# Kernel tuning notes

Measured on AMD Instinct MI355X. Metric: run time of the kernel, lower is better.

Reference implementation:

```python
import jax, jax.numpy as jnp
import numpy as np

DIM = 768
HEADS = 12
HEAD_DIM = DIM // HEADS


def setup_inputs() -> dict:
    key = jax.random.key(0)
    ks = jax.random.split(key, 5)
    s = 0.02
    return {
        "x": jax.random.normal(ks[0], (2, 4096, DIM), dtype=jnp.float32),
        "w_qkv": jax.random.normal(ks[1], (DIM, 3 * DIM), dtype=jnp.float32) * s,
        "b_qkv": jax.random.normal(ks[2], (3 * DIM,), dtype=jnp.float32) * s,
        "w_proj": jax.random.normal(ks[3], (DIM, DIM), dtype=jnp.float32) * s,
        "b_proj": jax.random.normal(ks[4], (DIM,), dtype=jnp.float32) * s,
    }


def reference(x, w_qkv, b_qkv, w_proj, b_proj):
    B, N, _ = x.shape
    scale = HEAD_DIM ** (-0.5)
    qkv = x @ w_qkv + b_qkv                              # [B, N, 3*DIM]
    q, k, v = jnp.split(qkv, 3, axis=-1)
    # 'b n (h d) -> b h n d'
    def to_heads(t):
        return t.reshape(B, N, HEADS, HEAD_DIM).transpose(0, 2, 1, 3)
    q, k, v = to_heads(q), to_heads(k), to_heads(v)
    attn = jnp.einsum('bhnd,bhmd->bhnm', q, k) * scale   # [B, H, N, N]
    attn = jax.nn.softmax(attn, axis=-1)
    out = jnp.einsum('bhnm,bhmd->bhnd', attn, v)         # [B, H, N, D]
    out = out.transpose(0, 2, 1, 3).reshape(B, N, DIM)   # 'b h n d -> b n (h d)'
    return out @ w_proj + b_proj
```

## Files before the change

### kernel.cpp

```cpp
#include <hip/hip_runtime.h>
#include <hip/hip_bf16.h>
#include <stdint.h>

typedef _Float16 f16x8 __attribute__((ext_vector_type(8)));
typedef _Float16 f16x4 __attribute__((ext_vector_type(4)));
typedef uint32_t u32x2 __attribute__((ext_vector_type(2)));
typedef uint32_t u32x4 __attribute__((ext_vector_type(4)));
typedef float floatx4 __attribute__((ext_vector_type(4)));

#define NSEQ 4096
#define DIMM 768
#define NHEADS 12
#define HD 64

__device__ __forceinline__ void gload_lds16(const void* g, void* l) {
  typedef __attribute__((address_space(1))) const uint32_t GQ;
  typedef __attribute__((address_space(3))) uint32_t LQ;
  __builtin_amdgcn_global_load_lds((GQ*)g, (LQ*)l, 16, 0, 0);
}

__device__ __forceinline__ uint16_t f16_bits(float v) {
  _Float16 h = (_Float16)v;
  return __builtin_bit_cast(uint16_t, h);
}

__device__ __forceinline__ uint32_t pkrtz(float a, float b) {
  return __builtin_bit_cast(uint32_t, __builtin_amdgcn_cvt_pkrtz(a, b));
}

__device__ __forceinline__ int swz(int row, int e) {
  return row * 64 + ((((e >> 3) ^ (row & 7)) << 3) | (e & 7));
}

__global__ __launch_bounds__(256) void prologue(
    const float* __restrict__ w0, const float* __restrict__ w1,
    uint16_t* __restrict__ d0, uint16_t* __restrict__ d1,
    const float4* __restrict__ xsrc, f16x8* __restrict__ xdst, int n8) {
  const int z = blockIdx.z;
  const int tx = threadIdx.x, ty = threadIdx.y;
  if (z == 2) {
    const int nthr = 72 * 24 * 256;
    int i = (blockIdx.y * 72 + blockIdx.x) * 256 + ty * 32 + tx;
    for (; i < n8; i += nthr) {
      const float4 a = xsrc[2 * i], b = xsrc[2 * i + 1];
      f16x8 o;
      o[0] = (_Float16)a.x; o[1] = (_Float16)a.y; o[2] = (_Float16)a.z; o[3] = (_Float16)a.w;
      o[4] = (_Float16)b.x; o[5] = (_Float16)b.y; o[6] = (_Float16)b.z; o[7] = (_Float16)b.w;
      xdst[i] = o;
    }
    return;
  }
  __shared__ uint16_t tile[32][33];
  if (z && blockIdx.x >= 24) return;
  const float* src = z ? w1 : w0;
  uint16_t* dst = z ? d1 : d0;
  const int C = z ? 768 : 2304;
  const int R = 768;
  const int c0 = blockIdx.x * 32, r0 = blockIdx.y * 32;
#pragma unroll
  for (int i = 0; i < 32; i += 8)
    tile[ty + i][tx] = f16_bits(src[(size_t)(r0 + ty + i) * C + (c0 + tx)]);
  __syncthreads();
#pragma unroll
  for (int i = 0; i < 32; i += 8)
    dst[(size_t)(c0 + ty + i) * R + (r0 + tx)] = tile[tx][ty + i];
}

__global__ __launch_bounds__(256) void gemm_bt(
    const _Float16* __restrict__ A, const _Float16* __restrict__ Bt,
    const float* __restrict__ bias, int K, int mode, int nbx,
    void* __restrict__ o0, _Float16* __restrict__ o1, _Float16* __restrict__ o2) {
  __shared__ __attribute__((aligned(16))) _Float16 As[3][128 * 32];
  __shared__ __attribute__((aligned(16))) _Float16 Bs[3][128 * 32];
  __shared__ float bias_s[128];
  const int tid = threadIdx.x;
  const int wv = tid >> 6;
  const int lane = tid & 63;
  const int quad = lane >> 4, l16 = lane & 15;
  const int wm = (wv >> 1) * 64, wn = (wv & 1) * 64;
  const int bid = blockIdx.x;
  const int xcd = bid & 7, idx = bid >> 3;
  const int by = xcd * 8 + (idx & 7);
  const int bx = idx >> 3;
  const int m0 = by * 128, n0 = bx * 128;
  (void)nbx;

  if (tid < 128) bias_s[tid] = bias[n0 + tid];

  floatx4 acc[4][4];
#pragma unroll
  for (int i = 0; i < 4; ++i)
#pragma unroll
    for (int j = 0; j < 4; ++j) acc[i][j] = (floatx4){0.f, 0.f, 0.f, 0.f};

  const int gr = lane >> 2, gc = (lane & 3) * 8;
  const _Float16* Ag = A + (size_t)(m0 + wv * 32 + gr) * K + gc;
  const _Float16* Bg = Bt + (size_t)(n0 + wv * 32 + gr) * K + gc;
  const size_t K16 = (size_t)16 * K;

  auto STAGE = [&](int buf, int kt) {
    _Float16* As0 = &As[buf][wv * 1024];
    _Float16* Bs0 = &Bs[buf][wv * 1024];
    gload_lds16(Ag + kt, As0);
    gload_lds16(Ag + kt + K16, As0 + 512);
    gload_lds16(Bg + kt, Bs0);
    gload_lds16(Bg + kt + K16, Bs0 + 512);
  };
  auto COMPUTE = [&](int buf) {
    f16x8 af[4], bfr[4];
#pragma unroll
    for (int i = 0; i < 4; ++i)
      af[i] = *(const f16x8*)&As[buf][(wm + i * 16 + l16) * 32 + quad * 8];
#pragma unroll
    for (int j = 0; j < 4; ++j)
      bfr[j] = *(const f16x8*)&Bs[buf][(wn + j * 16 + l16) * 32 + quad * 8];
    __builtin_amdgcn_s_setprio(1);
#pragma unroll
    for (int i = 0; i < 4; ++i)
#pragma unroll
      for (int j = 0; j < 4; ++j)
        acc[i][j] = __builtin_amdgcn_mfma_f32_16x16x32_f16(af[i], bfr[j], acc[i][j], 0, 0, 0);
    __builtin_amdgcn_s_setprio(0);
  };

  STAGE(0, 0);
  STAGE(1, 32);
  const int nt = K >> 5;
  int b0 = 0, b1 = 1, b2 = 2;
#pragma unroll 1
  for (int t = 0; t < nt - 2; ++t) {
    asm volatile("s_waitcnt vmcnt(4)" ::: "memory");
    __builtin_amdgcn_s_barrier();
    STAGE(b2, (t + 2) * 32);
    COMPUTE(b0);
    const int tmp = b0; b0 = b1; b1 = b2; b2 = tmp;
  }
  asm volatile("s_waitcnt vmcnt(4)" ::: "memory");
  __builtin_amdgcn_s_barrier();
  COMPUTE(b0);
  b0 = b1;
  asm volatile("s_waitcnt vmcnt(0)" ::: "memory");
  __builtin_amdgcn_s_barrier();
  COMPUTE(b0);

  if (mode == 0) {
    float* of = (float*)o0;
#pragma unroll
    for (int i = 0; i < 4; ++i)
#pragma unroll
      for (int j = 0; j < 4; ++j) {
        const int col = n0 + wn + j * 16 + l16;
        const float b = bias_s[wn + j * 16 + l16];
        const int mrow = m0 + wm + i * 16 + quad * 4;
#pragma unroll
        for (int r = 0; r < 4; ++r)
          of[(size_t)(mrow + r) * DIMM + col] = acc[i][j][r] + b;
      }
  } else {
    const int sec = n0 / DIMM;
    if (sec < 2) {
      _Float16* dst = (sec == 0) ? (_Float16*)o0 : o1;
      const float sc = (sec == 0) ? 0.18033688011112042f : 1.0f;
#pragma unroll
      for (int i = 0; i < 4; ++i)
#pragma unroll
        for (int j = 0; j < 4; ++j) {
          const int n = n0 + wn + j * 16 + l16;
          const int c = n - sec * DIMM;
          const int h = c >> 6, d = c & 63;
          const float b = bias_s[wn + j * 16 + l16];
          const int mrow = m0 + wm + i * 16 + quad * 4;
#pragma unroll
          for (int r = 0; r < 4; ++r) {
            const int m = mrow + r;
            const int bb = m >> 12, nr = m & 4095;
            dst[(((size_t)(bb * NHEADS + h)) * NSEQ + nr) * HD + d] =
                (_Float16)((acc[i][j][r] + b) * sc);
          }
        }
    } else {
#pragma unroll
      for (int i = 0; i < 4; ++i)
#pragma unroll
        for (int j = 0; j < 4; ++j) {
          const int c = n0 + wn + j * 16 + l16 - 2 * DIMM;
          const int h = c >> 6, d = c & 63;
          const float b = bias_s[wn + j * 16 + l16];
          const int mrow = m0 + wm + i * 16 + quad * 4;
          const int bb = mrow >> 12, nr = mrow & 4095;
          f16x4 v;
#pragma unroll
          for (int r = 0; r < 4; ++r) v[r] = (_Float16)(acc[i][j][r] + b);
          *(f16x4*)&o2[(((size_t)(bb * NHEADS + h)) * HD + d) * NSEQ + nr] = v;
        }
    }
  }
}

__global__ __launch_bounds__(256, 3) void attn(
    const _Float16* __restrict__ Qg, const _Float16* __restrict__ Kg,
    const _Float16* __restrict__ VTg, _Float16* __restrict__ ctx) {
  __shared__ __attribute__((aligned(16))) _Float16 Pt[128 * 64];
  __shared__ __attribute__((aligned(16))) _Float16 Ks[2][64 * 64];
  __shared__ __attribute__((aligned(16))) _Float16 VTs[2][64 * 64];
  const int tid = threadIdx.x;
  const int wv = tid >> 6, lane = tid & 63;
  const int quad = lane >> 4, l16 = lane & 15;
  const int bi = blockIdx.x;
  const int xcd = bi & 7, j = bi >> 3;
  const int bh = xcd * 3 + (j >> 5);
  const int q0 = (j & 31) * 128;
  const int bb = bh / NHEADS, h = bh - bb * NHEADS;
  const _Float16* Qp = Qg + (size_t)bh * NSEQ * HD;
  const _Float16* Kp = Kg + (size_t)bh * NSEQ * HD;
  const _Float16* VTp = VTg + (size_t)bh * HD * NSEQ;

  const int krow = tid >> 3;
  const int kcol = (((tid & 7) ^ ((tid >> 3) & 7)) * 8);

#pragma unroll
  for (int i = 0; i < 4; ++i)
    gload_lds16(Qp + (size_t)(q0 + i * 32 + krow) * HD + kcol, &Pt[(i * 256 + wv * 64) * 8]);
#pragma unroll
  for (int i = 0; i < 2; ++i) {
    gload_lds16(Kp + (size_t)(i * 32 + krow) * HD + kcol, &Ks[0][(i * 256 + wv * 64) * 8]);
    gload_lds16(VTp + (size_t)(i * 32 + krow) * NSEQ + kcol, &VTs[0][(i * 256 + wv * 64) * 8]);
  }
  __syncthreads();

  f16x8 aq[2][2];
#pragma unroll
  for (int it = 0; it < 2; ++it)
#pragma unroll
    for (int ks = 0; ks < 2; ++ks)
      aq[it][ks] = *(const f16x8*)&Pt[swz(wv * 32 + it * 16 + l16, ks * 32 + quad * 8)];

#pragma unroll
  for (int i = 0; i < 2; ++i) {
    gload_lds16(Kp + (size_t)(64 + i * 32 + krow) * HD + kcol, &Ks[1][(i * 256 + wv * 64) * 8]);
    gload_lds16(VTp + (size_t)(i * 32 + krow) * NSEQ + 64 + kcol, &VTs[1][(i * 256 + wv * 64) * 8]);
  }

  f16x8 ones;
#pragma unroll
  for (int e = 0; e < 8; ++e) ones[e] = (_Float16)1.0f;

  floatx4 o[2][4];
  floatx4 lacc[2];
#pragma unroll
  for (int it = 0; it < 2; ++it) {
    lacc[it] = (floatx4){0.f, 0.f, 0.f, 0.f};
#pragma unroll
    for (int jn = 0; jn < 4; ++jn) o[it][jn] = (floatx4){0.f, 0.f, 0.f, 0.f};
  }

  f16x8 vr[2][4];
  f16x8 ap[2][2];

  auto QKT = [&](const _Float16* bK, floatx4 (&s)[2][4]) {
#pragma unroll
    for (int ks = 0; ks < 2; ++ks) {
#pragma unroll
      for (int im = 0; im < 4; ++im) {
        const f16x8 bk = *(const f16x8*)&bK[swz(im * 16 + l16, ks * 32 + quad * 8)];
        s[0][im] = __builtin_amdgcn_mfma_f32_16x16x32_f16(bk, aq[0][ks], s[0][im], 0, 0, 0);
        s[1][im] = __builtin_amdgcn_mfma_f32_16x16x32_f16(bk, aq[1][ks], s[1][im], 0, 0, 0);
      }
    }
  };
  auto LDVR = [&](const _Float16* bV) {
#pragma unroll
    for (int kk = 0; kk < 2; ++kk)
#pragma unroll
      for (int jn = 0; jn < 4; ++jn)
        vr[kk][jn] = *(const f16x8*)&bV[swz(jn * 16 + l16, kk * 32 + quad * 8)];
  };
  auto SMAX = [&](floatx4 (&s)[2][4]) {
#pragma unroll
    for (int it = 0; it < 2; ++it) {
      uint32_t w[4][2];
#pragma unroll
      for (int im = 0; im < 4; ++im) {
        float p0 = __builtin_amdgcn_exp2f(s[it][im][0]);
        float p1 = __builtin_amdgcn_exp2f(s[it][im][1]);
        float p2 = __builtin_amdgcn_exp2f(s[it][im][2]);
        float p3 = __builtin_amdgcn_exp2f(s[it][im][3]);
        w[im][0] = pkrtz(p0, p1);
        w[im][1] = pkrtz(p2, p3);
      }
#pragma unroll
      for (int kk = 0; kk < 2; ++kk) {
        uint32_t a = w[2 * kk][0], c = w[2 * kk + 1][0];
        uint32_t b = w[2 * kk][1], d = w[2 * kk + 1][1];
        asm("v_permlane32_swap_b32 %0, %1" : "+v"(a), "+v"(c));
        asm("v_permlane16_swap_b32 %0, %1" : "+v"(a), "+v"(c));
        asm("v_permlane32_swap_b32 %0, %1" : "+v"(b), "+v"(d));
        asm("v_permlane16_swap_b32 %0, %1" : "+v"(b), "+v"(d));
        const u32x4 pk = {a, b, c, d};
        ap[kk][it] = __builtin_bit_cast(f16x8, pk);
      }
    }
  };
  auto PV = [&]() {
#pragma unroll
    for (int kk = 0; kk < 2; ++kk) {
      lacc[0] = __builtin_amdgcn_mfma_f32_16x16x32_f16(ap[kk][0], ones, lacc[0], 0, 0, 0);
      lacc[1] = __builtin_amdgcn_mfma_f32_16x16x32_f16(ap[kk][1], ones, lacc[1], 0, 0, 0);
#pragma unroll
      for (int jn = 0; jn < 4; ++jn) {
        o[0][jn] = __builtin_amdgcn_mfma_f32_16x16x32_f16(ap[kk][0], vr[kk][jn], o[0][jn], 0, 0, 0);
        o[1][jn] = __builtin_amdgcn_mfma_f32_16x16x32_f16(ap[kk][1], vr[kk][jn], o[1][jn], 0, 0, 0);
      }
    }
  };

  {
    floatx4 s[2][4];
#pragma unroll
    for (int it = 0; it < 2; ++it)
#pragma unroll
      for (int im = 0; im < 4; ++im) s[it][im] = (floatx4){0.f, 0.f, 0.f, 0.f};
    __builtin_amdgcn_s_setprio(1);
    QKT(Ks[0], s);
    __builtin_amdgcn_s_setprio(0);
    LDVR(VTs[0]);
    SMAX(s);
  }

  auto REGION = [&](const _Float16* bK, const _Float16* bV,
                    _Float16* wK, _Float16* wV, int kvn, bool dodma) {
    __syncthreads();
    if (dodma) {
#pragma unroll
      for (int i = 0; i < 2; ++i) {
        gload_lds16(Kp + (size_t)(kvn + i * 32 + krow) * HD + kcol, &wK[(i * 256 + wv * 64) * 8]);
        gload_lds16(VTp + (size_t)(i * 32 + krow) * NSEQ + kvn + kcol, &wV[(i * 256 + wv * 64) * 8]);
      }
    }
    floatx4 s[2][4];
#pragma unroll
    for (int it = 0; it < 2; ++it)
#pragma unroll
      for (int im = 0; im < 4; ++im) s[it][im] = (floatx4){0.f, 0.f, 0.f, 0.f};
    __builtin_amdgcn_s_setprio(1);
    QKT(bK, s);
    PV();
    __builtin_amdgcn_s_setprio(0);
    LDVR(bV);
    SMAX(s);
  };

#pragma unroll 1
  for (int p = 0; p < 31; ++p) {
    const int t0 = 2 * p + 1;
    REGION(Ks[1], VTs[1], Ks[0], VTs[0], (t0 + 1) * 64, true);
    REGION(Ks[0], VTs[0], Ks[1], VTs[1], (t0 + 2) * 64, true);
  }
  REGION(Ks[1], VTs[1], Ks[0], VTs[0], 0, false);
  PV();

#pragma unroll
  for (int it = 0; it < 2; ++it)
#pragma unroll
    for (int r = 0; r < 4; ++r) {
      const int q = q0 + wv * 32 + it * 16 + quad * 4 + r;
      const float inv = 1.0f / lacc[it][r];
      _Float16* dst = ctx + (size_t)(bb * NSEQ + q) * DIMM + h * HD;
#pragma unroll
      for (int jn = 0; jn < 4; ++jn)
        dst[jn * 16 + l16] = (_Float16)(o[it][jn][r] * inv);
    }
}

extern "C" void kernel_launch(void* const* d_in, const int* in_sizes, int n_in,
                              void* d_out, int out_size, void* d_ws, size_t ws_size,
                              hipStream_t stream) {
  char* ws = (char*)d_ws;
  _Float16* xc = (_Float16*)ws;      ws += (size_t)8192 * 768 * 2;
  _Float16* wqkvT = (_Float16*)ws;   ws += (size_t)2304 * 768 * 2;
  _Float16* wprojT = (_Float16*)ws;  ws += (size_t)768 * 768 * 2;
  const size_t qkv_elems = (size_t)2 * NHEADS * NSEQ * HD;
  _Float16* Qb = (_Float16*)ws;      ws += qkv_elems * 2;
  _Float16* Kb = (_Float16*)ws;      ws += qkv_elems * 2;
  _Float16* VTb = (_Float16*)ws;     ws += qkv_elems * 2;
  _Float16* ctx = xc;

  const dim3 tb(32, 8, 1);
  const dim3 b256(256, 1, 1);
  hipLaunchKernelGGL(prologue, dim3(72, 24, 3), tb, 0, stream,
                     (const float*)d_in[1], (const float*)d_in[3],
                     (uint16_t*)wqkvT, (uint16_t*)wprojT,
                     (const float4*)d_in[0], (f16x8*)xc, 8192 * 768 / 8);
  hipLaunchKernelGGL(gemm_bt, dim3(18 * 64, 1, 1), b256, 0, stream,
                     xc, wqkvT, (const float*)d_in[2], 768, 1, 18,
                     (void*)Qb, Kb, VTb);
  hipLaunchKernelGGL(attn, dim3(768, 1, 1), b256, 0, stream, Qb, Kb, VTb, ctx);
  hipLaunchKernelGGL(gemm_bt, dim3(6 * 64, 1, 1), b256, 0, stream,
                     ctx, wprojT, (const float*)d_in[4], 768, 0, 6, d_out,
                     (_Float16*)nullptr, (_Float16*)nullptr);
}
```

Before: 258.9 us.

## Split attention block across eight waves with sixteen query rows each

The attention kernel now runs 512 threads per block, so each of 8 waves owns 16 query rows instead of 4 waves owning 32. Q is staged through the K buffer instead of a dedicated LDS array, and each K/V tile is filled with one async load per thread. The aim is lower register use per wave, less LDS per block and more waves in flight to hide latency. In exchange, each K and V fragment read from LDS now feeds half as many MFMAs, roughly doubling LDS read traffic per unit of compute, and barriers now span more waves.

```diff
diff --git a/kernel.cpp b/kernel.cpp
--- a/kernel.cpp
+++ b/kernel.cpp
@@ -197,10 +197,9 @@
   }
 }
 
-__global__ __launch_bounds__(256, 3) void attn(
+__global__ __launch_bounds__(512, 6) void attn(
     const _Float16* __restrict__ Qg, const _Float16* __restrict__ Kg,
     const _Float16* __restrict__ VTg, _Float16* __restrict__ ctx) {
-  __shared__ __attribute__((aligned(16))) _Float16 Pt[128 * 64];
   __shared__ __attribute__((aligned(16))) _Float16 Ks[2][64 * 64];
   __shared__ __attribute__((aligned(16))) _Float16 VTs[2][64 * 64];
   const int tid = threadIdx.x;
@@ -218,53 +217,45 @@
   const int krow = tid >> 3;
   const int kcol = (((tid & 7) ^ ((tid >> 3) & 7)) * 8);
 
-#pragma unroll
-  for (int i = 0; i < 4; ++i)
-    gload_lds16(Qp + (size_t)(q0 + i * 32 + krow) * HD + kcol, &Pt[(i * 256 + wv * 64) * 8]);
-#pragma unroll
-  for (int i = 0; i < 2; ++i) {
-    gload_lds16(Kp + (size_t)(i * 32 + krow) * HD + kcol, &Ks[0][(i * 256 + wv * 64) * 8]);
-    gload_lds16(VTp + (size_t)(i * 32 + krow) * NSEQ + kcol, &VTs[0][(i * 256 + wv * 64) * 8]);
-  }
+  _Float16* qs = &Ks[0][0];
+#pragma unroll
+  for (int i = 0; i < 2; ++i)
+    gload_lds16(Qp + (size_t)(q0 + i * 64 + krow) * HD + kcol, &qs[(i * 512 + wv * 64) * 8]);
   __syncthreads();
 
-  f16x8 aq[2][2];
-#pragma unroll
-  for (int it = 0; it < 2; ++it)
-#pragma unroll
-    for (int ks = 0; ks < 2; ++ks)
-      aq[it][ks] = *(const f16x8*)&Pt[swz(wv * 32 + it * 16 + l16, ks * 32 + quad * 8)];
-
-#pragma unroll
-  for (int i = 0; i < 2; ++i) {
-    gload_lds16(Kp + (size_t)(64 + i * 32 + krow) * HD + kcol, &Ks[1][(i * 256 + wv * 64) * 8]);
-    gload_lds16(VTp + (size_t)(i * 32 + krow) * NSEQ + 64 + kcol, &VTs[1][(i * 256 + wv * 64) * 8]);
-  }
+  f16x8 aq[2];
+#pragma unroll
+  for (int ks = 0; ks < 2; ++ks)
+    aq[ks] = *(const f16x8*)&qs[swz(wv * 16 + l16, ks * 32 + quad * 8)];
+  __syncthreads();
+
+  auto GDMA = [&](int kvn, _Float16* wK, _Float16* wV) {
+    gload_lds16(Kp + (size_t)(kvn + krow) * HD + kcol, &wK[(wv * 64) * 8]);
+    gload_lds16(VTp + (size_t)krow * NSEQ + kvn + kcol, &wV[(wv * 64) * 8]);
+  };
+  GDMA(0, Ks[0], VTs[0]);
+  GDMA(64, Ks[1], VTs[1]);
+  __syncthreads();
 
   f16x8 ones;
 #pragma unroll
   for (int e = 0; e < 8; ++e) ones[e] = (_Float16)1.0f;
 
-  floatx4 o[2][4];
-  floatx4 lacc[2];
-#pragma unroll
-  for (int it = 0; it < 2; ++it) {
-    lacc[it] = (floatx4){0.f, 0.f, 0.f, 0.f};
-#pragma unroll
-    for (int jn = 0; jn < 4; ++jn) o[it][jn] = (floatx4){0.f, 0.f, 0.f, 0.f};
-  }
+  floatx4 o[4];
+  floatx4 lacc = (floatx4){0.f, 0.f, 0.f, 0.f};
+#pragma unroll
+  for (int jn = 0; jn < 4; ++jn) o[jn] = (floatx4){0.f, 0.f, 0.f, 0.f};
 
   f16x8 vr[2][4];
-  f16x8 ap[2][2];
-
-  auto QKT = [&](const _Float16* bK, floatx4 (&s)[2][4]) {
+  f16x8 ap[2];
+
+  auto QKT = [&](const _Float16* bK, floatx4 (&s)[4]) {
 #pragma unroll
     for (int ks = 0; ks < 2; ++ks) {
 #pragma unroll
       for (int im = 0; im < 4; ++im) {
         const f16x8 bk = *(const f16x8*)&bK[swz(im * 16 + l16, ks * 32 + quad * 8)];
-        s[0][im] = __builtin_amdgcn_mfma_f32_16x16x32_f16(bk, aq[0][ks], s[0][im], 0, 0, 0);
-        s[1][im] = __builtin_amdgcn_mfma_f32_16x16x32_f16(bk, aq[1][ks], s[1][im], 0, 0, 0);
+        s[im] = __builtin_amdgcn_mfma_f32_16x16x32_f16(bk, aq[ks], s[im], 0, 0, 0);
       }
     }
   };
@@ -275,51 +266,43 @@
       for (int jn = 0; jn < 4; ++jn)
         vr[kk][jn] = *(const f16x8*)&bV[swz(jn * 16 + l16, kk * 32 + quad * 8)];
   };
-  auto SMAX = [&](floatx4 (&s)[2][4]) {
-#pragma unroll
-    for (int it = 0; it < 2; ++it) {
-      uint32_t w[4][2];
-#pragma unroll
-      for (int im = 0; im < 4; ++im) {
-        float p0 = __builtin_amdgcn_exp2f(s[it][im][0]);
-        float p1 = __builtin_amdgcn_exp2f(s[it][im][1]);
-        float p2 = __builtin_amdgcn_exp2f(s[it][im][2]);
-        float p3 = __builtin_amdgcn_exp2f(s[it][im][3]);
-        w[im][0] = pkrtz(p0, p1);
-        w[im][1] = pkrtz(p2, p3);
-      }
-#pragma unroll
-      for (int kk = 0; kk < 2; ++kk) {
-        uint32_t a = w[2 * kk][0], c = w[2 * kk + 1][0];
-        uint32_t b = w[2 * kk][1], d = w[2 * kk + 1][1];
-        asm("v_permlane32_swap_b32 %0, %1" : "+v"(a), "+v"(c));
-        asm("v_permlane16_swap_b32 %0, %1" : "+v"(a), "+v"(c));
-        asm("v_permlane32_swap_b32 %0, %1" : "+v"(b), "+v"(d));
-        asm("v_permlane16_swap_b32 %0, %1" : "+v"(b), "+v"(d));
-        const u32x4 pk = {a, b, c, d};
-        ap[kk][it] = __builtin_bit_cast(f16x8, pk);
-      }
+  auto SMAX = [&](floatx4 (&s)[4]) {
+    uint32_t w[4][2];
+#pragma unroll
+    for (int im = 0; im < 4; ++im) {
+      float p0 = __builtin_amdgcn_exp2f(s[im][0]);
+      float p1 = __builtin_amdgcn_exp2f(s[im][1]);
+      float p2 = __builtin_amdgcn_exp2f(s[im][2]);
+      float p3 = __builtin_amdgcn_exp2f(s[im][3]);
+      w[im][0] = pkrtz(p0, p1);
+      w[im][1] = pkrtz(p2, p3);
+    }
+#pragma unroll
+    for (int kk = 0; kk < 2; ++kk) {
+      uint32_t a = w[2 * kk][0], c = w[2 * kk + 1][0];
+      uint32_t b = w[2 * kk][1], d = w[2 * kk + 1][1];
+      asm("v_permlane32_swap_b32 %0, %1" : "+v"(a), "+v"(c));
+      asm("v_permlane16_swap_b32 %0, %1" : "+v"(a), "+v"(c));
+      asm("v_permlane32_swap_b32 %0, %1" : "+v"(b), "+v"(d));
+      asm("v_permlane16_swap_b32 %0, %1" : "+v"(b), "+v"(d));
+      const u32x4 pk = {a, b, c, d};
+      ap[kk] = __builtin_bit_cast(f16x8, pk);
     }
   };
   auto PV = [&]() {
 #pragma unroll
     for (int kk = 0; kk < 2; ++kk) {
-      lacc[0] = __builtin_amdgcn_mfma_f32_16x16x32_f16(ap[kk][0], ones, lacc[0], 0, 0, 0);
-      lacc[1] = __builtin_amdgcn_mfma_f32_16x16x32_f16(ap[kk][1], ones, lacc[1], 0, 0, 0);
-#pragma unroll
-      for (int jn = 0; jn < 4; ++jn) {
-        o[0][jn] = __builtin_amdgcn_mfma_f32_16x16x32_f16(ap[kk][0], vr[kk][jn], o[0][jn], 0, 0, 0);
-        o[1][jn] = __builtin_amdgcn_mfma_f32_16x16x32_f16(ap[kk][1], vr[kk][jn], o[1][jn], 0, 0, 0);
-      }
+      lacc = __builtin_amdgcn_mfma_f32_16x16x32_f16(ap[kk], ones, lacc, 0, 0, 0);
+#pragma unroll
+      for (int jn = 0; jn < 4; ++jn)
+        o[jn] = __builtin_amdgcn_mfma_f32_16x16x32_f16(ap[kk], vr[kk][jn], o[jn], 0, 0, 0);
     }
   };
 
   {
-    floatx4 s[2][4];
-#pragma unroll
-    for (int it = 0; it < 2; ++it)
-#pragma unroll
-      for (int im = 0; im < 4; ++im) s[it][im] = (floatx4){0.f, 0.f, 0.f, 0.f};
+    floatx4 s[4];
+#pragma unroll
+    for (int im = 0; im < 4; ++im) s[im] = (floatx4){0.f, 0.f, 0.f, 0.f};
     __builtin_amdgcn_s_setprio(1);
     QKT(Ks[0], s);
     __builtin_amdgcn_s_setprio(0);
@@ -330,18 +313,10 @@
   auto REGION = [&](const _Float16* bK, const _Float16* bV,
                     _Float16* wK, _Float16* wV, int kvn, bool dodma) {
     __syncthreads();
-    if (dodma) {
-#pragma unroll
-      for (int i = 0; i < 2; ++i) {
-        gload_lds16(Kp + (size_t)(kvn + i * 32 + krow) * HD + kcol, &wK[(i * 256 + wv * 64) * 8]);
-        gload_lds16(VTp + (size_t)(i * 32 + krow) * NSEQ + kvn + kcol, &wV[(i * 256 + wv * 64) * 8]);
-      }
-    }
-    floatx4 s[2][4];
-#pragma unroll
-    for (int it = 0; it < 2; ++it)
-#pragma unroll
-      for (int im = 0; im < 4; ++im) s[it][im] = (floatx4){0.f, 0.f, 0.f, 0.f};
+    if (dodma) GDMA(kvn, wK, wV);
+    floatx4 s[4];
+#pragma unroll
+    for (int im = 0; im < 4; ++im) s[im] = (floatx4){0.f, 0.f, 0.f, 0.f};
     __builtin_amdgcn_s_setprio(1);
     QKT(bK, s);
     PV();
@@ -360,16 +335,14 @@
   PV();
 
 #pragma unroll
-  for (int it = 0; it < 2; ++it)
-#pragma unroll
-    for (int r = 0; r < 4; ++r) {
-      const int q = q0 + wv * 32 + it * 16 + quad * 4 + r;
-      const float inv = 1.0f / lacc[it][r];
-      _Float16* dst = ctx + (size_t)(bb * NSEQ + q) * DIMM + h * HD;
-#pragma unroll
-      for (int jn = 0; jn < 4; ++jn)
-        dst[jn * 16 + l16] = (_Float16)(o[it][jn][r] * inv);
-    }
+  for (int r = 0; r < 4; ++r) {
+    const int q = q0 + wv * 16 + quad * 4 + r;
+    const float inv = 1.0f / lacc[r];
+    _Float16* dst = ctx + (size_t)(bb * NSEQ + q) * DIMM + h * HD;
+#pragma unroll
+    for (int jn = 0; jn < 4; ++jn)
+      dst[jn * 16 + l16] = (_Float16)(o[jn][r] * inv);
+  }
 }
 
 extern "C" void kernel_launch(void* const* d_in, const int* in_sizes, int n_in,
@@ -394,7 +367,8 @@
   hipLaunchKernelGGL(gemm_bt, dim3(18 * 64, 1, 1), b256, 0, stream,
                      xc, wqkvT, (const float*)d_in[2], 768, 1, 18,
                      (void*)Qb, Kb, VTb);
-  hipLaunchKernelGGL(attn, dim3(768, 1, 1), b256, 0, stream, Qb, Kb, VTb, ctx);
+  hipLaunchKernelGGL(attn, dim3(768, 1, 1), dim3(512, 1, 1), 0, stream,
+                     Qb, Kb, VTb, ctx);
   hipLaunchKernelGGL(gemm_bt, dim3(6 * 64, 1, 1), b256, 0, stream,
                      ctx, wprojT, (const float*)d_in[4], 768, 0, 6, d_out,
                      (_Float16*)nullptr, (_Float16*)nullptr);
```

New measurement: 1.000 ms. 286% more time.
